# Optimization experiments

Measured on AMD Instinct MI355X. Metric: run time of the kernel, lower is better.

## Reference

```python
import jax, jax.numpy as jnp
import numpy as np

LAMBDA = 20.0   # lambda_val (blackbox-diff smoothing)
REG = 0.5       # reg
MAX_LABEL = 8   # labels drawn in [0, MAX_LABEL)


def _pairwise_dist(x):
    # x: [n, d] -> [n, n] euclidean distances (safe sqrt, exact 0 on diagonal)
    sq = jnp.sum(x * x, axis=-1)
    d2 = sq[:, None] + sq[None, :] - 2.0 * (x @ x.T)
    d2 = jnp.maximum(d2, 0.0)
    return jnp.where(d2 > 0, jnp.sqrt(jnp.where(d2 > 0, d2, 1.0)), 0.0)


def _single_linkage_adj(D, k):
    # Agglomerative (single-linkage) clustering of n points given [n,n] dists,
    # stopped at k clusters; returns [n,n] 0/1 cluster-adjacency matrix.
    n = D.shape[0]
    BIG = jnp.asarray(1e9, D.dtype)
    eye = jnp.eye(n, dtype=bool)
    Dw0 = jnp.where(eye, BIG, D)
    labels0 = jnp.arange(n)
    active0 = jnp.ones((n,), dtype=bool)

    def step(carry, _):
        Dw, labels, active = carry
        mask = active[:, None] & active[None, :] & ~eye
        flat = jnp.argmin(jnp.where(mask, Dw, BIG))
        i, j = flat // n, flat % n
        a = jnp.minimum(i, j)
        b = jnp.maximum(i, j)
        newrow = jnp.minimum(Dw[a], Dw[b])        # single linkage merge
        Dw = Dw.at[a, :].set(newrow).at[:, a].set(newrow)
        active = active.at[b].set(False)
        labels = jnp.where(labels == b, a, labels)
        return (Dw, labels, active), labels

    _, hist = jax.lax.scan(step, (Dw0, labels0, active0), None, length=n - 1)
    all_hist = jnp.concatenate([labels0[None, :], hist], axis=0)  # [n, n]; row m = labels after m merges (n-m clusters)
    lab = all_hist[n - k]
    return (lab[:, None] == lab[None, :]).astype(D.dtype)


def _solve(dists, ks):
    return jax.vmap(_single_linkage_adj)(dists, ks)


def setup_inputs() -> dict:
    key = jax.random.key(0)
    k1, k2, k3 = jax.random.split(key, 3)
    B, n, d = 256, 64, 768
    return {
        "query_embedding": jax.random.normal(k1, (B, d), dtype=jnp.float32),
        "psg_embeddings": jax.random.normal(k2, (B, n, d), dtype=jnp.float32),
        "labels": jax.random.randint(k3, (B, n), 0, MAX_LABEL, dtype=jnp.int64)
        if jax.config.jax_enable_x64 else jax.random.randint(k3, (B, n), 0, MAX_LABEL, dtype=jnp.int32),
    }


def reference(query_embedding, psg_embeddings, labels):
    # true_adj_mat: adj[i,j] = 1 iff i==j or label[i]==label[j] (diag is label-equal anyway)
    true_adj = (labels[:, :, None] == labels[:, None, :]).astype(jnp.float32)  # [B,n,n]
    # ks[i] = number of unique labels in sample i
    presence = (labels[..., None] == jnp.arange(MAX_LABEL)).any(axis=1)  # [B, MAX_LABEL]
    ks = presence.sum(axis=-1)

    scaled = query_embedding[:, None, :] * psg_embeddings            # [B,n,d]
    dists = jax.vmap(_pairwise_dist)(scaled)                          # [B,n,n]

    mean_similar = (dists * true_adj).sum() / true_adj.sum()
    mean_dissimilar = (dists * (1.0 - true_adj)).sum() / (1.0 - true_adj).sum()

    adj = _solve(dists, ks)                                           # OptimCluster forward
    err = adj * (1.0 - true_adj) + (1.0 - adj) * true_adj
    err_mean = err.mean(axis=0).sum()
    return err_mean + REG * (mean_similar - mean_dissimilar)
```

## Files before the change

### kernel.cpp

```cpp
#include <hip/hip_runtime.h>


#define NPTS 64
#define DIM 768
#define CH 128
#define NCH 6
#define NT 512
#define BIGF 1e9f
#define PGS 68

typedef __attribute__((ext_vector_type(8))) __bf16 bf16x8;
typedef __attribute__((ext_vector_type(4))) float f32x4;
typedef __attribute__((ext_vector_type(8))) unsigned short us8;

__device__ __forceinline__ void lds_fence() {
  asm volatile("s_waitcnt lgkmcnt(0)" ::: "memory");
  __builtin_amdgcn_sched_barrier(0);
}

__device__ __forceinline__ void split2(float x, unsigned short& h,
                                       unsigned short& m) {
  unsigned u = __float_as_uint(x);
  unsigned rb = (u + 0x7FFFu + ((u >> 16) & 1u)) & 0xFFFF0000u;
  h = (unsigned short)(rb >> 16);
  float r1 = x - __uint_as_float(rb);
  unsigned u1 = __float_as_uint(r1);
  unsigned rb1 = (u1 + 0x7FFFu + ((u1 >> 16) & 1u)) & 0xFFFF0000u;
  m = (unsigned short)(rb1 >> 16);
}

__device__ __forceinline__ void publish6(int v, unsigned long long (&m)[6]) {
  #pragma unroll
  for (int k = 0; k < 6; ++k) m[k] = __ballot(((v >> k) & 1) != 0);
}
__device__ __forceinline__ int extract6(const unsigned long long (&m)[6], int p) {
  int r = 0;
  #pragma unroll
  for (int k = 0; k < 6; ++k) r |= (int)((m[k] >> p) & 1ull) << k;
  return r;
}
__device__ __forceinline__ unsigned long long match6(int v) {
  unsigned long long m = ~0ull;
  #pragma unroll
  for (int bb = 0; bb < 6; ++bb) {
    unsigned long long mb = __ballot(((v >> bb) & 1) != 0);
    m &= (((v >> bb) & 1) != 0) ? mb : ~mb;
  }
  return m;
}

__device__ __forceinline__ void stage_chunk(
    unsigned short (*Hb)[NPTS][CH], const float4 (&pva)[2][2],
    const float4 (&qv)[2], int row0, int gran) {
  #pragma unroll
  for (int rr = 0; rr < 2; ++rr) {
    const int row = row0 + (rr << 5);
    float xs[8];
    xs[0] = pva[rr][0].x * qv[0].x; xs[1] = pva[rr][0].y * qv[0].y;
    xs[2] = pva[rr][0].z * qv[0].z; xs[3] = pva[rr][0].w * qv[0].w;
    xs[4] = pva[rr][1].x * qv[1].x; xs[5] = pva[rr][1].y * qv[1].y;
    xs[6] = pva[rr][1].z * qv[1].z; xs[7] = pva[rr][1].w * qv[1].w;
    us8 uh, um;
    #pragma unroll
    for (int e = 0; e < 8; ++e) {
      unsigned short hh, mm;
      split2(xs[e], hh, mm);
      uh[e] = hh; um[e] = mm;
    }
    const int p = gran ^ (row & 15);
    *reinterpret_cast<us8*>(&Hb[0][row][p << 3]) = uh;
    *reinterpret_cast<us8*>(&Hb[1][row][p << 3]) = um;
  }
}

__device__ __forceinline__ void mfma_chunk(
    const unsigned short (*Hb)[NPTS][CH], f32x4 (&acc)[2][2],
    int R, int C, int ksub, int lrow, int lhi) {
  #pragma unroll 1
  for (int ss = 0; ss < 2; ++ss) {
    const int s = ksub + (ss << 1);
    const int p = ((s << 2) + lhi) ^ lrow;
    bf16x8 fa[2][2], fb[2][2];
    #pragma unroll
    for (int v = 0; v < 2; ++v)
      #pragma unroll
      for (int tb = 0; tb < 2; ++tb) {
        const int row = (R << 5) + (tb << 4) + lrow;
        fa[v][tb] = *reinterpret_cast<const bf16x8*>(&Hb[v][row][p << 3]);
      }
    if (R != C) {
      #pragma unroll
      for (int v = 0; v < 2; ++v)
        #pragma unroll
        for (int tb = 0; tb < 2; ++tb) {
          const int row = (C << 5) + (tb << 4) + lrow;
          fb[v][tb] = *reinterpret_cast<const bf16x8*>(&Hb[v][row][p << 3]);
        }
    } else {
      #pragma unroll
      for (int v = 0; v < 2; ++v)
        #pragma unroll
        for (int tb = 0; tb < 2; ++tb) fb[v][tb] = fa[v][tb];
    }
    #pragma unroll
    for (int ti = 0; ti < 2; ++ti)
      #pragma unroll
      for (int tj = 0; tj < 2; ++tj) {
        acc[ti][tj] = __builtin_amdgcn_mfma_f32_16x16x32_bf16(fa[0][ti], fb[0][tj], acc[ti][tj], 0, 0, 0);
        acc[ti][tj] = __builtin_amdgcn_mfma_f32_16x16x32_bf16(fa[0][ti], fb[1][tj], acc[ti][tj], 0, 0, 0);
        acc[ti][tj] = __builtin_amdgcn_mfma_f32_16x16x32_bf16(fa[1][ti], fb[0][tj], acc[ti][tj], 0, 0, 0);
        acc[ti][tj] = __builtin_amdgcn_mfma_f32_16x16x32_bf16(fa[1][ti], fb[1][tj], acc[ti][tj], 0, 0, 0);
      }
  }
}

#define ISSUE_P(PV, cix) do {                                       \
    const int off_ = (cix) * CH;                                    \
    PV[0][0] = *(const float4*)(pr0 + off_);                        \
    PV[0][1] = *(const float4*)(pr0 + off_ + 4);                    \
    PV[1][0] = *(const float4*)(pr1 + off_);                        \
    PV[1][1] = *(const float4*)(pr1 + off_ + 4);                    \
  } while (0)

#define ISSUE_Q(QV, cix) do {                                       \
    const int off_ = (cix) * CH;                                    \
    QV[0] = *(const float4*)(qr + off_);                            \
    QV[1] = *(const float4*)(qr + off_ + 4);                        \
  } while (0)

__global__ __launch_bounds__(NT) void fused_kernel(
    const float* __restrict__ q,
    const float* __restrict__ psg,
    const int*   __restrict__ labels,
    float* __restrict__ simS_o, float* __restrict__ disS_o,
    int* __restrict__ simC_o, int* __restrict__ errC_o)
{
  __shared__ __align__(16) unsigned short Hml[2][2][NPTS][CH];
  __shared__ __align__(16) float PG[NPTS * PGS];
  __shared__ float diagf[NPTS];
  __shared__ int lab_s[NPTS];
  __shared__ __align__(8) unsigned long long ekey_s[NPTS];

  const int b = blockIdx.x;
  const int t = threadIdx.x;
  const int w = t >> 6;
  const int l = t & 63;

  const float* qb = q + (size_t)b * DIM;
  const float* pb = psg + (size_t)b * NPTS * DIM;

  const int row0 = t >> 4;
  const int gran = t & 15;
  const float* pr0 = pb + (size_t)row0 * DIM + (gran << 3);
  const float* pr1 = pr0 + 32 * DIM;
  const float* qr  = qb + (gran << 3);

  const int rw = w >> 1;
  const int R = rw >> 1, C = rw & 1;
  const int ksub = w & 1;
  const int lrow = l & 15;
  const int lhi  = l >> 4;

  f32x4 acc[2][2];
  {
    f32x4 z = {0.f, 0.f, 0.f, 0.f};
    acc[0][0] = z; acc[0][1] = z; acc[1][0] = z; acc[1][1] = z;
  }

  float4 pvaA[2][2], pvaB[2][2], qv[2];

  ISSUE_P(pvaA, 0);
  ISSUE_Q(qv, 0);
  ISSUE_P(pvaB, 1);
  stage_chunk(Hml[0], pvaA, qv, row0, gran);
  __syncthreads();

  #pragma unroll 1
  for (int cc = 0; cc < 3; ++cc) {
    if (cc < 2) ISSUE_P(pvaA, 2 * cc + 2);
    ISSUE_Q(qv, 2 * cc + 1);
    mfma_chunk(Hml[0], acc, R, C, ksub, lrow, lhi);
    stage_chunk(Hml[1], pvaB, qv, row0, gran);
    __syncthreads();
    if (cc < 2) {
      ISSUE_P(pvaB, 2 * cc + 3);
      ISSUE_Q(qv, 2 * cc + 2);
    }
    mfma_chunk(Hml[1], acc, R, C, ksub, lrow, lhi);
    if (cc < 2) stage_chunk(Hml[0], pvaA, qv, row0, gran);
    __syncthreads();
  }

  if (w & 1) {
    float* dst = PG + (rw << 10);
    #pragma unroll
    for (int ti = 0; ti < 2; ++ti)
      #pragma unroll
      for (int tj = 0; tj < 2; ++tj)
        *reinterpret_cast<f32x4*>(dst + (((ti << 1) + tj) << 8) + (l << 2)) = acc[ti][tj];
  }
  __syncthreads();
  if (!(w & 1)) {
    const float* src = PG + (rw << 10);
    #pragma unroll
    for (int ti = 0; ti < 2; ++ti)
      #pragma unroll
      for (int tj = 0; tj < 2; ++tj)
        acc[ti][tj] += *reinterpret_cast<const f32x4*>(src + (((ti << 1) + tj) << 8) + (l << 2));
  }
  __syncthreads();
  if (!(w & 1)) {
    #pragma unroll
    for (int ti = 0; ti < 2; ++ti)
      #pragma unroll
      for (int tj = 0; tj < 2; ++tj)
        #pragma unroll
        for (int reg = 0; reg < 4; ++reg) {
          const int grow = (R << 5) + (ti << 4) + (lhi << 2) + reg;
          const int gcol = (C << 5) + (tj << 4) + lrow;
          const float gv = acc[ti][tj][reg];
          PG[grow * PGS + gcol] = gv;
          if (grow == gcol) diagf[grow] = gv;
        }
  }
  __syncthreads();

  {
    const int r  = t >> 3;
    const int c0 = (t & 7) << 3;
    const float dr = diagf[r];
    #pragma unroll
    for (int e = 0; e < 8; ++e) {
      const int cc = c0 + e;
      const float gg = PG[r * PGS + cc];
      float d2 = dr + diagf[cc] - 2.f * gg;
      d2 = fmaxf(d2, 0.f);
      PG[r * PGS + cc] = (d2 > 0.f) ? sqrtf(d2) : 0.f;
    }
  }
  __syncthreads();
  if (w != 0) return;

  float drow[64];
  #pragma unroll
  for (int v4 = 0; v4 < 16; ++v4) {
    f32x4 x = *reinterpret_cast<const f32x4*>(&PG[l * PGS + (v4 << 2)]);
    drow[v4 * 4 + 0] = x[0]; drow[v4 * 4 + 1] = x[1];
    drow[v4 * 4 + 2] = x[2]; drow[v4 * 4 + 3] = x[3];
  }
  int tl = labels[b * NPTS + l];

  unsigned long long sMask = 0ull;
  int kcnt = 0;
  #pragma unroll
  for (int v = 0; v < 8; ++v) {
    unsigned long long mv = __ballot(tl == v);
    kcnt += (mv != 0ull) ? 1 : 0;
    if (tl == v) sMask = mv;
  }
  int simC = __popcll(sMask);
  const int merges = NPTS - kcnt;

  float simS = 0.f, disS = 0.f;
  #pragma unroll
  for (int j = 0; j < NPTS; ++j) {
    bool sim = (sMask >> j) & 1ull;
    simS += sim ? drow[j] : 0.f;
    disS += sim ? 0.f : drow[j];
  }

  unsigned long long same = 1ull << l;
  int repSlot = l;
  int ecnt = 0;

  #pragma unroll 1
  for (int rd = 0; rd < 6; ++rd) {
    float bva = BIGF, bvb = BIGF, bvc = BIGF, bvd = BIGF;
    int bja = 64, bjb = 64, bjc = 64, bjd = 64;
    #pragma unroll
    for (int j4 = 0; j4 < 16; ++j4) {
      const int j = j4 << 2;
      bool oa = !((same >> (j + 0)) & 1ull) && (drow[j + 0] < bva);
      bva = oa ? drow[j + 0] : bva; bja = oa ? j + 0 : bja;
      bool ob = !((same >> (j + 1)) & 1ull) && (drow[j + 1] < bvb);
      bvb = ob ? drow[j + 1] : bvb; bjb = ob ? j + 1 : bjb;
      bool oc = !((same >> (j + 2)) & 1ull) && (drow[j + 2] < bvc);
      bvc = oc ? drow[j + 2] : bvc; bjc = oc ? j + 2 : bjc;
      bool od = !((same >> (j + 3)) & 1ull) && (drow[j + 3] < bvd);
      bvd = od ? drow[j + 3] : bvd; bjd = od ? j + 3 : bjd;
    }
    float bv = bva; int bj = bja;
    if (bvb < bv || (bvb == bv && bjb < bj)) { bv = bvb; bj = bjb; }
    if (bvc < bv || (bvc == bv && bjc < bj)) { bv = bvc; bj = bjc; }
    if (bvd < bv || (bvd == bv && bjd < bj)) { bv = bvd; bj = bjd; }

    const unsigned bits = (bj < 64) ? __float_as_uint(bv) : 0xFFFFFFFFu;
    unsigned long long cand = same;
    unsigned minb = 0u;
    #pragma unroll
    for (int k = 31; k >= 0; --k) {
      unsigned long long mb = __ballot(((bits >> k) & 1u) != 0u);
      unsigned long long z = cand & ~mb;
      bool hz = (z != 0ull);
      cand = hz ? z : cand;
      minb = (minb << 1) | (hz ? 0u : 1u);
    }
    const bool valid = (minb != 0xFFFFFFFFu);
    const int wl = __ffsll((long long)cand) - 1;

    unsigned long long bjm[6]; publish6(bj, bjm);
    const int v_wl = extract6(bjm, wl);

    unsigned long long rpm[6]; publish6(repSlot, rpm);
    const int otherRep = extract6(rpm, v_wl);

    const bool isRoot = (l == repSlot);
    int ptr = repSlot;
    if (isRoot && valid) ptr = otherRep;

    unsigned long long pm[6]; publish6(ptr, pm);
    const int pd = extract6(pm, ptr);
    bool adder = false;
    if (isRoot && valid && ptr != l) {
      if (pd == l && l < ptr) ptr = l;
      else adder = true;
    }
    const unsigned long long A = __ballot(adder);
    if (adder)
      ekey_s[ecnt + __popcll(A & ((1ull << l) - 1ull))] =
          ((unsigned long long)minb << 12) |
          (unsigned long long)((wl << 6) | v_wl);
    ecnt += (int)__popcll(A);

    #pragma unroll 1
    for (int jj = 0; jj < 6; ++jj) {
      unsigned long long dm[6]; publish6(ptr, dm);
      const int p2 = extract6(dm, ptr);
      if (__ballot(p2 != ptr) == 0ull) break;
      ptr = p2;
    }
    same = match6(ptr);
    repSlot = __ffsll((long long)same) - 1;
    if (same == ~0ull) break;
  }
  lds_fence();

  const bool ehave = (l < ecnt);
  const unsigned long long my = ehave ? ekey_s[l] : ~0ull;
  int rank = 0;
  #pragma unroll 7
  for (int j = 0; j < 63; ++j) {
    unsigned long long kj = ekey_s[j];
    rank += (j < ecnt && kj < my) ? 1 : 0;
  }
  const bool kept = ehave && (rank < merges);
  const int eu = (int)((my >> 6) & 63);
  const int ev = (int)(my & 63);

  lab_s[l] = l;
  lds_fence();
  #pragma unroll 1
  for (int iter = 0; iter < 64; ++iter) {
    int m = 0; bool ch = false;
    if (kept) {
      const int lu = lab_s[eu], lv = lab_s[ev];
      m = min(lu, lv);
      ch = (m < lu) || (m < lv);
    }
    if (ch) {
      atomicMin(&lab_s[eu], m);
      atomicMin(&lab_s[ev], m);
    }
    lds_fence();
    const int la = lab_s[l];
    const int lb = lab_s[la];
    if (lb < la) lab_s[l] = lb;
    lds_fence();
    if (__ballot(ch) == 0ull) break;
  }
  const int cl = lab_s[l];

  const unsigned long long cMask = match6(cl);
  int ec2 = __popcll(cMask ^ sMask);

  #pragma unroll
  for (int off = 32; off; off >>= 1) {
    simS += __shfl_xor(simS, off);
    disS += __shfl_xor(disS, off);
    simC += __shfl_xor(simC, off);
    ec2  += __shfl_xor(ec2, off);
  }
  if (l == 0) {
    simS_o[b] = simS; disS_o[b] = disS;
    simC_o[b] = simC; errC_o[b] = ec2;
  }
}

__global__ __launch_bounds__(64) void finalize_kernel(
    const float* __restrict__ simS, const float* __restrict__ disS,
    const int* __restrict__ simC, const int* __restrict__ errC,
    float* __restrict__ out)
{
  const int l = threadIdx.x;
  double ss = 0.0, dd = 0.0, sc = 0.0, ec = 0.0;
  #pragma unroll
  for (int r = 0; r < 4; ++r) {
    int i = (r << 6) + l;
    ss += (double)simS[i];
    dd += (double)disS[i];
    sc += (double)simC[i];
    ec += (double)errC[i];
  }
  #pragma unroll
  for (int off = 32; off; off >>= 1) {
    ss += __shfl_xor(ss, off);
    dd += __shfl_xor(dd, off);
    sc += __shfl_xor(sc, off);
    ec += __shfl_xor(ec, off);
  }
  if (l == 0) {
    const double total = 256.0 * 4096.0;
    double ms = ss / sc;
    double md = dd / (total - sc);
    out[0] = (float)(ec / 256.0 + 0.5 * (ms - md));
  }
}

extern "C" void kernel_launch(void* const* d_in, const int* in_sizes, int n_in,
                              void* d_out, int out_size, void* d_ws, size_t ws_size,
                              hipStream_t stream) {
  const float* q      = (const float*)d_in[0];
  const float* psg    = (const float*)d_in[1];
  const int*   labels = (const int*)d_in[2];
  float* out = (float*)d_out;

  float* simS = (float*)d_ws;
  float* disS = simS + 256;
  int*   simC = (int*)(disS + 256);
  int*   errC = simC + 256;

  fused_kernel<<<256, NT, 0, stream>>>(q, psg, labels, simS, disS, simC, errC);
  finalize_kernel<<<1, 64, 0, stream>>>(simS, disS, simC, errC, out);
}
```

Baseline: 32.34 us.

## Double block size to 1024 threads, splitting K across four waves per tile

Raises the thread count per block from 512 to 1024. Each thread now stages one row per chunk, and each output tile's K dimension is split over four waves (one k-substep each) instead of two. The partial accumulators are combined with a two-level reduction through the reused Hml LDS buffer. This aims to hide global-load and MFMA latency with more waves per block, at the cost of an extra reduction step and sync and of fewer resident blocks per CU. The later single-wave clustering phase is unchanged, so the extra waves sit idle there.

```diff
diff --git a/kernel.cpp b/kernel.cpp
--- a/kernel.cpp
+++ b/kernel.cpp
@@ -5,7 +5,7 @@
 #define DIM 768
 #define CH 128
 #define NCH 6
-#define NT 512
+#define NT 1024
 #define BIGF 1e9f
 #define PGS 68
 
@@ -50,76 +50,66 @@
 }
 
 __device__ __forceinline__ void stage_chunk(
-    unsigned short (*Hb)[NPTS][CH], const float4 (&pva)[2][2],
-    const float4 (&qv)[2], int row0, int gran) {
-  #pragma unroll
-  for (int rr = 0; rr < 2; ++rr) {
-    const int row = row0 + (rr << 5);
-    float xs[8];
-    xs[0] = pva[rr][0].x * qv[0].x; xs[1] = pva[rr][0].y * qv[0].y;
-    xs[2] = pva[rr][0].z * qv[0].z; xs[3] = pva[rr][0].w * qv[0].w;
-    xs[4] = pva[rr][1].x * qv[1].x; xs[5] = pva[rr][1].y * qv[1].y;
-    xs[6] = pva[rr][1].z * qv[1].z; xs[7] = pva[rr][1].w * qv[1].w;
-    us8 uh, um;
-    #pragma unroll
-    for (int e = 0; e < 8; ++e) {
-      unsigned short hh, mm;
-      split2(xs[e], hh, mm);
-      uh[e] = hh; um[e] = mm;
-    }
-    const int p = gran ^ (row & 15);
-    *reinterpret_cast<us8*>(&Hb[0][row][p << 3]) = uh;
-    *reinterpret_cast<us8*>(&Hb[1][row][p << 3]) = um;
-  }
+    unsigned short (*Hb)[NPTS][CH], const float4 (&pva)[2],
+    const float4 (&qv)[2], int row, int gran) {
+  float xs[8];
+  xs[0] = pva[0].x * qv[0].x; xs[1] = pva[0].y * qv[0].y;
+  xs[2] = pva[0].z * qv[0].z; xs[3] = pva[0].w * qv[0].w;
+  xs[4] = pva[1].x * qv[1].x; xs[5] = pva[1].y * qv[1].y;
+  xs[6] = pva[1].z * qv[1].z; xs[7] = pva[1].w * qv[1].w;
+  us8 uh, um;
+  #pragma unroll
+  for (int e = 0; e < 8; ++e) {
+    unsigned short hh, mm;
+    split2(xs[e], hh, mm);
+    uh[e] = hh; um[e] = mm;
+  }
+  const int p = gran ^ (row & 15);
+  *reinterpret_cast<us8*>(&Hb[0][row][p << 3]) = uh;
+  *reinterpret_cast<us8*>(&Hb[1][row][p << 3]) = um;
 }
 
 __device__ __forceinline__ void mfma_chunk(
     const unsigned short (*Hb)[NPTS][CH], f32x4 (&acc)[2][2],
-    int R, int C, int ksub, int lrow, int lhi) {
-  #pragma unroll 1
-  for (int ss = 0; ss < 2; ++ss) {
-    const int s = ksub + (ss << 1);
-    const int p = ((s << 2) + lhi) ^ lrow;
-    bf16x8 fa[2][2], fb[2][2];
+    int R, int C, int s, int lrow, int lhi) {
+  const int p = ((s << 2) + lhi) ^ lrow;
+  bf16x8 fa[2][2], fb[2][2];
+  #pragma unroll
+  for (int v = 0; v < 2; ++v)
+    #pragma unroll
+    for (int tb = 0; tb < 2; ++tb) {
+      const int row = (R << 5) + (tb << 4) + lrow;
+      fa[v][tb] = *reinterpret_cast<const bf16x8*>(&Hb[v][row][p << 3]);
+    }
+  if (R != C) {
     #pragma unroll
     for (int v = 0; v < 2; ++v)
       #pragma unroll
       for (int tb = 0; tb < 2; ++tb) {
-        const int row = (R << 5) + (tb << 4) + lrow;
-        fa[v][tb] = *reinterpret_cast<const bf16x8*>(&Hb[v][row][p << 3]);
+        const int row = (C << 5) + (tb << 4) + lrow;
+        fb[v][tb] = *reinterpret_cast<const bf16x8*>(&Hb[v][row][p << 3]);
       }
-    if (R != C) {
-      #pragma unroll
-      for (int v = 0; v < 2; ++v)
-        #pragma unroll
-        for (int tb = 0; tb < 2; ++tb) {
-          const int row = (C << 5) + (tb << 4) + lrow;
-          fb[v][tb] = *reinterpret_cast<const bf16x8*>(&Hb[v][row][p << 3]);
-        }
-    } else {
-      #pragma unroll
-      for (int v = 0; v < 2; ++v)
-        #pragma unroll
-        for (int tb = 0; tb < 2; ++tb) fb[v][tb] = fa[v][tb];
-    }
-    #pragma unroll
-    for (int ti = 0; ti < 2; ++ti)
-      #pragma unroll
-      for (int tj = 0; tj < 2; ++tj) {
-        acc[ti][tj] = __builtin_amdgcn_mfma_f32_16x16x32_bf16(fa[0][ti], fb[0][tj], acc[ti][tj], 0, 0, 0);
-        acc[ti][tj] = __builtin_amdgcn_mfma_f32_16x16x32_bf16(fa[0][ti], fb[1][tj], acc[ti][tj], 0, 0, 0);
-        acc[ti][tj] = __builtin_amdgcn_mfma_f32_16x16x32_bf16(fa[1][ti], fb[0][tj], acc[ti][tj], 0, 0, 0);
-        acc[ti][tj] = __builtin_amdgcn_mfma_f32_16x16x32_bf16(fa[1][ti], fb[1][tj], acc[ti][tj], 0, 0, 0);
-      }
-  }
+  } else {
+    #pragma unroll
+    for (int v = 0; v < 2; ++v)
+      #pragma unroll
+      for (int tb = 0; tb < 2; ++tb) fb[v][tb] = fa[v][tb];
+  }
+  #pragma unroll
+  for (int ti = 0; ti < 2; ++ti)
+    #pragma unroll
+    for (int tj = 0; tj < 2; ++tj) {
+      acc[ti][tj] = __builtin_amdgcn_mfma_f32_16x16x32_bf16(fa[0][ti], fb[0][tj], acc[ti][tj], 0, 0, 0);
+      acc[ti][tj] = __builtin_amdgcn_mfma_f32_16x16x32_bf16(fa[0][ti], fb[1][tj], acc[ti][tj], 0, 0, 0);
+      acc[ti][tj] = __builtin_amdgcn_mfma_f32_16x16x32_bf16(fa[1][ti], fb[0][tj], acc[ti][tj], 0, 0, 0);
+      acc[ti][tj] = __builtin_amdgcn_mfma_f32_16x16x32_bf16(fa[1][ti], fb[1][tj], acc[ti][tj], 0, 0, 0);
+    }
 }
 
 #define ISSUE_P(PV, cix) do {                                       \
     const int off_ = (cix) * CH;                                    \
-    PV[0][0] = *(const float4*)(pr0 + off_);                        \
-    PV[0][1] = *(const float4*)(pr0 + off_ + 4);                    \
-    PV[1][0] = *(const float4*)(pr1 + off_);                        \
-    PV[1][1] = *(const float4*)(pr1 + off_ + 4);                    \
+    PV[0] = *(const float4*)(pr + off_);                            \
+    PV[1] = *(const float4*)(pr + off_ + 4);                        \
   } while (0)
 
 #define ISSUE_Q(QV, cix) do {                                       \
@@ -151,13 +141,12 @@
 
   const int row0 = t >> 4;
   const int gran = t & 15;
-  const float* pr0 = pb + (size_t)row0 * DIM + (gran << 3);
-  const float* pr1 = pr0 + 32 * DIM;
-  const float* qr  = qb + (gran << 3);
-
-  const int rw = w >> 1;
+  const float* pr = pb + (size_t)row0 * DIM + (gran << 3);
+  const float* qr = qb + (gran << 3);
+
+  const int rw = w >> 2;
   const int R = rw >> 1, C = rw & 1;
-  const int ksub = w & 1;
+  const int ksub = w & 3;
   const int lrow = l & 15;
   const int lhi  = l >> 4;
 
@@ -167,7 +156,7 @@
     acc[0][0] = z; acc[0][1] = z; acc[1][0] = z; acc[1][1] = z;
   }
 
-  float4 pvaA[2][2], pvaB[2][2], qv[2];
+  float4 pvaA[2], pvaB[2], qv[2];
 
   ISSUE_P(pvaA, 0);
   ISSUE_Q(qv, 0);
@@ -191,8 +180,9 @@
     __syncthreads();
   }
 
-  if (w & 1) {
-    float* dst = PG + (rw << 10);
+  float* scr = (float*)&Hml[0][0][0][0];
+  if (ksub >= 2) {
+    float* dst = scr + (((rw << 1) | (ksub & 1)) << 10);
     #pragma unroll
     for (int ti = 0; ti < 2; ++ti)
       #pragma unroll
@@ -200,16 +190,30 @@
         *reinterpret_cast<f32x4*>(dst + (((ti << 1) + tj) << 8) + (l << 2)) = acc[ti][tj];
   }
   __syncthreads();
-  if (!(w & 1)) {
-    const float* src = PG + (rw << 10);
+  if (ksub < 2) {
+    const float* src = scr + (((rw << 1) | ksub) << 10);
     #pragma unroll
     for (int ti = 0; ti < 2; ++ti)
       #pragma unroll
       for (int tj = 0; tj < 2; ++tj)
         acc[ti][tj] += *reinterpret_cast<const f32x4*>(src + (((ti << 1) + tj) << 8) + (l << 2));
+    if (ksub == 1) {
+      float* dst = scr + ((8 + rw) << 10);
+      #pragma unroll
+      for (int ti = 0; ti < 2; ++ti)
+        #pragma unroll
+        for (int tj = 0; tj < 2; ++tj)
+          *reinterpret_cast<f32x4*>(dst + (((ti << 1) + tj) << 8) + (l << 2)) = acc[ti][tj];
+    }
   }
   __syncthreads();
-  if (!(w & 1)) {
+  if (ksub == 0) {
+    const float* src = scr + ((8 + rw) << 10);
+    #pragma unroll
+    for (int ti = 0; ti < 2; ++ti)
+      #pragma unroll
+      for (int tj = 0; tj < 2; ++tj)
+        acc[ti][tj] += *reinterpret_cast<const f32x4*>(src + (((ti << 1) + tj) << 8) + (l << 2));
     #pragma unroll
     for (int ti = 0; ti < 2; ++ti)
       #pragma unroll
@@ -226,11 +230,11 @@
   __syncthreads();
 
   {
-    const int r  = t >> 3;
-    const int c0 = (t & 7) << 3;
+    const int r  = t >> 4;
+    const int c0 = (t & 15) << 2;
     const float dr = diagf[r];
     #pragma unroll
-    for (int e = 0; e < 8; ++e) {
+    for (int e = 0; e < 4; ++e) {
       const int cc = c0 + e;
       const float gg = PG[r * PGS + cc];
       float d2 = dr + diagf[cc] - 2.f * gg;
```

New measurement: 32.11 us. Within noise of the previous version (-0.7%).

## Triple-buffer LDS staging and deepen prefetch of embedding chunks

Applied to the files above, without the earlier changes.

The six-chunk Gram accumulation now uses three LDS buffers instead of two and is fully unrolled. Global loads for the next chunks (two in flight, with separate q registers) are issued earlier, so the MFMA work on one buffer overlaps staging into another and load latency is better hidden. The split-K reduction scratch moves from PG into the now-idle Hml buffers, which removes one __syncthreads. The cost is more LDS (about 32KB extra for the third buffer) and more live registers, which may reduce occupancy.

```diff
diff --git a/kernel.cpp b/kernel.cpp
--- a/kernel.cpp
+++ b/kernel.cpp
@@ -4,7 +4,6 @@
 #define NPTS 64
 #define DIM 768
 #define CH 128
-#define NCH 6
 #define NT 512
 #define BIGF 1e9f
 #define PGS 68
@@ -135,7 +134,7 @@
     float* __restrict__ simS_o, float* __restrict__ disS_o,
     int* __restrict__ simC_o, int* __restrict__ errC_o)
 {
-  __shared__ __align__(16) unsigned short Hml[2][2][NPTS][CH];
+  __shared__ __align__(16) unsigned short Hml[3][2][NPTS][CH];
   __shared__ __align__(16) float PG[NPTS * PGS];
   __shared__ float diagf[NPTS];
   __shared__ int lab_s[NPTS];
@@ -167,32 +166,38 @@
     acc[0][0] = z; acc[0][1] = z; acc[1][0] = z; acc[1][1] = z;
   }
 
-  float4 pvaA[2][2], pvaB[2][2], qv[2];
-
-  ISSUE_P(pvaA, 0);
-  ISSUE_Q(qv, 0);
-  ISSUE_P(pvaB, 1);
-  stage_chunk(Hml[0], pvaA, qv, row0, gran);
-  __syncthreads();
-
-  #pragma unroll 1
-  for (int cc = 0; cc < 3; ++cc) {
-    if (cc < 2) ISSUE_P(pvaA, 2 * cc + 2);
-    ISSUE_Q(qv, 2 * cc + 1);
-    mfma_chunk(Hml[0], acc, R, C, ksub, lrow, lhi);
-    stage_chunk(Hml[1], pvaB, qv, row0, gran);
-    __syncthreads();
-    if (cc < 2) {
-      ISSUE_P(pvaB, 2 * cc + 3);
-      ISSUE_Q(qv, 2 * cc + 2);
-    }
-    mfma_chunk(Hml[1], acc, R, C, ksub, lrow, lhi);
-    if (cc < 2) stage_chunk(Hml[0], pvaA, qv, row0, gran);
-    __syncthreads();
-  }
-
+  float4 pvaA[2][2], pvaB[2][2], qvA[2], qvB[2];
+
+  ISSUE_P(pvaA, 0); ISSUE_Q(qvA, 0);
+  ISSUE_P(pvaB, 1); ISSUE_Q(qvB, 1);
+  stage_chunk(Hml[0], pvaA, qvA, row0, gran);
+  ISSUE_P(pvaA, 2); ISSUE_Q(qvA, 2);
+  stage_chunk(Hml[1], pvaB, qvB, row0, gran);
+  ISSUE_P(pvaB, 3); ISSUE_Q(qvB, 3);
+  __syncthreads();
+
+  mfma_chunk(Hml[0], acc, R, C, ksub, lrow, lhi);
+  stage_chunk(Hml[2], pvaA, qvA, row0, gran);
+  ISSUE_P(pvaA, 4); ISSUE_Q(qvA, 4);
+  __syncthreads();
+  mfma_chunk(Hml[1], acc, R, C, ksub, lrow, lhi);
+  stage_chunk(Hml[0], pvaB, qvB, row0, gran);
+  ISSUE_P(pvaB, 5); ISSUE_Q(qvB, 5);
+  __syncthreads();
+  mfma_chunk(Hml[2], acc, R, C, ksub, lrow, lhi);
+  stage_chunk(Hml[1], pvaA, qvA, row0, gran);
+  __syncthreads();
+  mfma_chunk(Hml[0], acc, R, C, ksub, lrow, lhi);
+  stage_chunk(Hml[2], pvaB, qvB, row0, gran);
+  __syncthreads();
+  mfma_chunk(Hml[1], acc, R, C, ksub, lrow, lhi);
+  __syncthreads();
+  mfma_chunk(Hml[2], acc, R, C, ksub, lrow, lhi);
+  __syncthreads();
+
+  float* scr = (float*)&Hml[0][0][0][0];
   if (w & 1) {
-    float* dst = PG + (rw << 10);
+    float* dst = scr + (rw << 10);
     #pragma unroll
     for (int ti = 0; ti < 2; ++ti)
       #pragma unroll
@@ -201,15 +206,12 @@
   }
   __syncthreads();
   if (!(w & 1)) {
-    const float* src = PG + (rw << 10);
+    const float* src = scr + (rw << 10);
     #pragma unroll
     for (int ti = 0; ti < 2; ++ti)
       #pragma unroll
       for (int tj = 0; tj < 2; ++tj)
         acc[ti][tj] += *reinterpret_cast<const f32x4*>(src + (((ti << 1) + tj) << 8) + (l << 2));
-  }
-  __syncthreads();
-  if (!(w & 1)) {
     #pragma unroll
     for (int ti = 0; ti < 2; ++ti)
       #pragma unroll
```

Result: no change. 32.19 us (-0.5%).
